# Kernel optimization log

Hardware: AMD Instinct MI355X
Metric: run time of the kernel (lower is better)

## Reference

```python
import jax, jax.numpy as jnp
import numpy as np

N_NODES = 50000
N_EDGES = 640000
HIDDEN = 128
N_LAYERS = 4
NUM_RBF = 50
CUTOFF = 4.0
N_GRAPHS = 64
VOCAB = 128
LN_EPS = 1e-5


def setup_inputs() -> dict:
    key = jax.random.key(0)
    ks = jax.random.split(key, 16)
    s = 1.0 / np.sqrt(HIDDEN)
    sr = 1.0 / np.sqrt(NUM_RBF)
    inp = {
        "x": jax.random.randint(ks[0], (N_NODES,), 0, VOCAB, dtype=jnp.int64) if jax.config.jax_enable_x64 else jax.random.randint(ks[0], (N_NODES,), 0, VOCAB).astype(jnp.int32),
        "edge_index": jax.random.randint(ks[1], (2, N_EDGES), 0, N_NODES).astype(jnp.int32),
        "edge_attr": jax.random.uniform(ks[2], (N_EDGES,), dtype=jnp.float32) * CUTOFF,
        "batch": jnp.sort(jax.random.randint(ks[3], (N_NODES,), 0, N_GRAPHS)).astype(jnp.int32),
        # embedding table
        "emb": jax.random.normal(ks[4], (VOCAB, HIDDEN), dtype=jnp.float32),
        # filter net: Linear(num_rbf, H) -> ReLU -> Linear(H, H), stacked over layers
        "fw1": jax.random.normal(ks[5], (N_LAYERS, NUM_RBF, HIDDEN), dtype=jnp.float32) * sr,
        "fb1": jnp.zeros((N_LAYERS, HIDDEN), dtype=jnp.float32),
        "fw2": jax.random.normal(ks[6], (N_LAYERS, HIDDEN, HIDDEN), dtype=jnp.float32) * s,
        "fb2": jnp.zeros((N_LAYERS, HIDDEN), dtype=jnp.float32),
        # lin: Linear(H, H) per layer
        "lw": jax.random.normal(ks[7], (N_LAYERS, HIDDEN, HIDDEN), dtype=jnp.float32) * s,
        "lb": jnp.zeros((N_LAYERS, HIDDEN), dtype=jnp.float32),
        # LayerNorm params per layer
        "ln_g": jnp.ones((N_LAYERS, HIDDEN), dtype=jnp.float32),
        "ln_b": jnp.zeros((N_LAYERS, HIDDEN), dtype=jnp.float32),
    }
    return inp


def _gaussian_smearing(dist):
    offset = jnp.linspace(0.0, CUTOFF, NUM_RBF, dtype=jnp.float32)  # [R]
    coeff = -0.5 / (CUTOFF / (NUM_RBF - 1)) ** 2
    d = dist[:, None] - offset[None, :]  # [E, R]
    return jnp.exp(coeff * d * d)


def _layer_norm(h, g, b):
    mu = jnp.mean(h, axis=-1, keepdims=True)
    var = jnp.mean(jnp.square(h - mu), axis=-1, keepdims=True)
    return (h - mu) * jax.lax.rsqrt(var + LN_EPS) * g + b


def reference(x, edge_index, edge_attr, batch, emb, fw1, fb1, fw2, fb2, lw, lb, ln_g, ln_b):
    edge_rbf = _gaussian_smearing(edge_attr)          # [E, R]
    h = emb[x]                                        # [N, H]
    row, col = edge_index[0], edge_index[1]
    for i in range(N_LAYERS):
        # FilterNet(RBF): [E, H]
        w = jax.nn.relu(edge_rbf @ fw1[i] + fb1[i]) @ fw2[i] + fb2[i]
        xl = h @ lw[i] + lb[i]                        # [N, H]
        msg = xl[col] * w                             # gather + elementwise, [E, H]
        out = jax.ops.segment_sum(msg, row, num_segments=N_NODES)
        h = _layer_norm(h + out, ln_g[i], ln_b[i])
    # global mean pool over graphs
    sums = jax.ops.segment_sum(h, batch, num_segments=N_GRAPHS)      # [G, H]
    cnt = jax.ops.segment_sum(jnp.ones((N_NODES,), h.dtype), batch, num_segments=N_GRAPHS)
    return sums / jnp.maximum(cnt, 1.0)[:, None]
```

## Files before the change

### kernel.cpp

```cpp
#include <hip/hip_runtime.h>
#include <hip/hip_bf16.h>

#define N_NODES 50000
#define N_EDGES 640000
#define HIDDEN 128
#define N_LAYERS 4
#define NUM_RBF 50
#define CUTOFF 4.0f
#define N_GRAPHS 64
#define TAB 8192
#define TG 8
#define PSPLIT 16
#define COLBITS 17

typedef unsigned int uint;
typedef unsigned short ushort;
typedef __attribute__((ext_vector_type(8))) short bf16x8;
typedef __attribute__((ext_vector_type(4))) float f32x4;

__device__ inline ushort f2bf(float f) {
    uint u = __float_as_uint(f);
    uint r = (u + 0x7fffu + ((u >> 16) & 1u)) >> 16;
    return (ushort)r;
}
__device__ inline uint packbf(float lo, float hi) {
    return (uint)f2bf(lo) | ((uint)f2bf(hi) << 16);
}
__device__ inline float bflo(uint u) { return __uint_as_float(u << 16); }
__device__ inline float bfhi(uint u) { return __uint_as_float(u & 0xffff0000u); }

__global__ __launch_bounds__(128) void k_table(const float* __restrict__ fw1,
                                               const float* __restrict__ fb1,
                                               const float* __restrict__ fw2,
                                               const float* __restrict__ fb2,
                                               uint* __restrict__ ctab) {
    int bid = blockIdx.x;
    int layer = bid / (TAB / TG);
    int g0 = (bid % (TAB / TG)) * TG;
    int j = threadIdx.x;
    __shared__ float rbf[TG][NUM_RBF];
    __shared__ float wout[TG][HIDDEN];
    __shared__ float hid[TG][HIDDEN];
    for (int idx = j; idx < TG * NUM_RBF; idx += 128) {
        int gg = idx / NUM_RBF, r = idx % NUM_RBF;
        float d = (CUTOFF * (g0 + gg)) / (float)(TAB - 1);
        float offset = (CUTOFF * r) / (float)(NUM_RBF - 1);
        float delta = CUTOFF / (float)(NUM_RBF - 1);
        float coeff = -0.5f / (delta * delta);
        float t = d - offset;
        rbf[gg][r] = expf(coeff * t * t);
    }
    __syncthreads();
    const float* w1 = fw1 + layer * NUM_RBF * HIDDEN;
    float b1 = fb1[layer * HIDDEN + j];
    float acc[TG];
    #pragma unroll
    for (int gg = 0; gg < TG; gg++) acc[gg] = b1;
    for (int r = 0; r < NUM_RBF; r++) {
        float w = w1[r * HIDDEN + j];
        #pragma unroll
        for (int gg = 0; gg < TG; gg++) acc[gg] = fmaf(rbf[gg][r], w, acc[gg]);
    }
    #pragma unroll
    for (int gg = 0; gg < TG; gg++) hid[gg][j] = fmaxf(acc[gg], 0.0f);
    __syncthreads();
    const float* w2 = fw2 + layer * HIDDEN * HIDDEN;
    float b2 = fb2[layer * HIDDEN + j];
    float acc2[TG];
    #pragma unroll
    for (int gg = 0; gg < TG; gg++) acc2[gg] = b2;
    for (int k = 0; k < HIDDEN; k += 4) {
        float w0 = w2[(k + 0) * HIDDEN + j];
        float w1v = w2[(k + 1) * HIDDEN + j];
        float w2v = w2[(k + 2) * HIDDEN + j];
        float w3 = w2[(k + 3) * HIDDEN + j];
        #pragma unroll
        for (int gg = 0; gg < TG; gg++) {
            acc2[gg] = fmaf(hid[gg][k + 0], w0, acc2[gg]);
            acc2[gg] = fmaf(hid[gg][k + 1], w1v, acc2[gg]);
            acc2[gg] = fmaf(hid[gg][k + 2], w2v, acc2[gg]);
            acc2[gg] = fmaf(hid[gg][k + 3], w3, acc2[gg]);
        }
    }
    #pragma unroll
    for (int gg = 0; gg < TG; gg++) wout[gg][j] = acc2[gg];
    __syncthreads();
    for (int idx = j; idx < TG * 64; idx += 128) {
        int gg = idx >> 6, jp = idx & 63;
        ctab[((size_t)layer * TAB + g0 + gg) * 64 + jp] =
            packbf(wout[gg][2 * jp], wout[gg][2 * jp + 1]);
    }
}

__global__ void k_embed(const int* __restrict__ x, const float* __restrict__ emb,
                        ushort* __restrict__ hbf) {
    int idx = blockIdx.x * 256 + threadIdx.x;
    if (idx >= N_NODES * 32) return;
    int n = idx >> 5, q = idx & 31;
    float4 v = ((const float4*)emb)[x[n] * 32 + q];
    uint2 p;
    p.x = packbf(v.x, v.y);
    p.y = packbf(v.z, v.w);
    ((uint2*)hbf)[idx] = p;
}

__global__ void k_packw(const float* __restrict__ lw, uint4* __restrict__ pb) {
    int idx = blockIdx.x * 256 + threadIdx.x;
    if (idx >= N_LAYERS * 8 * 4 * 64) return;
    int lane = idx & 63;
    int kc = (idx >> 6) & 3;
    int nt = (idx >> 8) & 7;
    int layer = idx >> 11;
    int quad = lane >> 4, nl = lane & 15;
    int n = nt * 16 + nl;
    const float* w = lw + layer * HIDDEN * HIDDEN;
    uint r[4];
    #pragma unroll
    for (int jj = 0; jj < 4; jj++) {
        int k = kc * 32 + quad * 8 + 2 * jj;
        r[jj] = packbf(w[k * HIDDEN + n], w[(k + 1) * HIDDEN + n]);
    }
    uint4 o; o.x = r[0]; o.y = r[1]; o.z = r[2]; o.w = r[3];
    pb[idx] = o;
}

__global__ void k_count(const int* __restrict__ row, int* __restrict__ counts) {
    int e = blockIdx.x * 256 + threadIdx.x;
    if (e < N_EDGES) atomicAdd(&counts[row[e]], 1);
}

__global__ void k_scan1(const int* __restrict__ counts, int* __restrict__ partial,
                        int* __restrict__ blocksum) {
    int i = blockIdx.x * 256 + threadIdx.x;
    int v = (i < N_NODES) ? counts[i] : 0;
    int lane = threadIdx.x & 63;
    int wid = threadIdx.x >> 6;
    int s = v;
    #pragma unroll
    for (int off = 1; off < 64; off <<= 1) {
        int t = __shfl_up(s, off, 64);
        if (lane >= off) s += t;
    }
    __shared__ int wsum[4];
    if (lane == 63) wsum[wid] = s;
    __syncthreads();
    int woff = 0;
    for (int w = 0; w < wid; w++) woff += wsum[w];
    int incl = s + woff;
    if (i < N_NODES) partial[i] = incl - v;
    if (threadIdx.x == 255) blocksum[blockIdx.x] = incl;
}

__global__ void k_scan2(int* __restrict__ blocksum, int nblk) {
    int tid = threadIdx.x;
    int v = (tid < nblk) ? blocksum[tid] : 0;
    int lane = tid & 63, wid = tid >> 6;
    int s = v;
    #pragma unroll
    for (int off = 1; off < 64; off <<= 1) {
        int t = __shfl_up(s, off, 64);
        if (lane >= off) s += t;
    }
    __shared__ int wsum[4];
    if (lane == 63) wsum[wid] = s;
    __syncthreads();
    int woff = 0;
    for (int w = 0; w < wid; w++) woff += wsum[w];
    int incl = s + woff;
    if (tid < nblk) blocksum[tid] = incl - v;
}

__global__ void k_scan3(const int* __restrict__ partial, const int* __restrict__ blocksum,
                        int* __restrict__ offsets, int* __restrict__ cursor) {
    int i = blockIdx.x * 256 + threadIdx.x;
    if (i < N_NODES) {
        int o = partial[i] + blocksum[blockIdx.x];
        offsets[i] = o;
        cursor[i] = o;
    }
    if (i == 0) offsets[N_NODES] = N_EDGES;
}

__global__ void k_fill(const int* __restrict__ row, const int* __restrict__ col,
                       const float* __restrict__ eattr, int* __restrict__ cursor,
                       uint* __restrict__ meta) {
    int e = blockIdx.x * 256 + threadIdx.x;
    if (e >= N_EDGES) return;
    int r = row[e];
    int pos = atomicAdd(&cursor[r], 1);
    float t = eattr[e] * ((float)(TAB - 1) / CUTOFF);
    int gi = (int)(t + 0.5f);
    gi = min(max(gi, 0), TAB - 1);
    meta[pos] = (uint)col[e] | ((uint)gi << COLBITS);
}

__global__ __launch_bounds__(256) void k_xl(const ushort* __restrict__ hbf,
                                            const uint4* __restrict__ pb,
                                            const float* __restrict__ lb,
                                            ushort* __restrict__ xlb) {
    int wave = threadIdx.x >> 6, lane = threadIdx.x & 63;
    int m0 = (blockIdx.x * 4 + wave) * 16;
    if (m0 >= N_NODES) return;
    int quad = lane >> 4, ml = lane & 15;
    const ushort* arow = hbf + (size_t)(m0 + ml) * HIDDEN + quad * 8;
    bf16x8 a[4];
    #pragma unroll
    for (int kc = 0; kc < 4; kc++) a[kc] = *(const bf16x8*)(arow + kc * 32);
    #pragma unroll
    for (int nt = 0; nt < 8; nt++) {
        f32x4 acc = {0.f, 0.f, 0.f, 0.f};
        #pragma unroll
        for (int kc = 0; kc < 4; kc++) {
            bf16x8 b = *(const bf16x8*)(pb + (nt * 4 + kc) * 64 + lane);
            acc = __builtin_amdgcn_mfma_f32_16x16x32_bf16(a[kc], b, acc, 0, 0, 0);
        }
        int col = nt * 16 + ml;
        float bias = lb[col];
        #pragma unroll
        for (int r = 0; r < 4; r++) {
            int row = m0 + quad * 4 + r;
            xlb[(size_t)row * HIDDEN + col] = f2bf(acc[r] + bias);
        }
    }
}

__global__ __launch_bounds__(256) void k_agg(const ushort* __restrict__ xlb,
                                             const uint* __restrict__ meta,
                                             const int* __restrict__ offsets,
                                             const uint* __restrict__ ctab,
                                             const ushort* __restrict__ hb_in,
                                             const float* __restrict__ g,
                                             const float* __restrict__ b,
                                             ushort* __restrict__ hbf_out) {
    int wid = threadIdx.x >> 6;
    int lane = threadIdx.x & 63;
    int n = blockIdx.x * 4 + wid;
    if (n >= N_NODES) return;
    const uint* xl2 = (const uint*)xlb;
    float accx = 0.f, accy = 0.f;
    int p0 = offsets[n], p1 = offsets[n + 1];
    int cnt = p1 - p0;
    for (int base = 0; base < cnt; base += 64) {
        int li = p0 + base + lane;
        uint mlv = meta[min(li, N_EDGES - 1)];
        int kk = min(64, cnt - base);
        int k4 = kk & ~3;
        int p = 0;
        for (; p < k4; p += 4) {
            uint m0 = __builtin_amdgcn_readlane(mlv, p + 0);
            uint m1 = __builtin_amdgcn_readlane(mlv, p + 1);
            uint m2 = __builtin_amdgcn_readlane(mlv, p + 2);
            uint m3 = __builtin_amdgcn_readlane(mlv, p + 3);
            uint w0 = ctab[(m0 >> COLBITS) * 64 + lane];
            uint w1 = ctab[(m1 >> COLBITS) * 64 + lane];
            uint w2 = ctab[(m2 >> COLBITS) * 64 + lane];
            uint w3 = ctab[(m3 >> COLBITS) * 64 + lane];
            uint x0 = xl2[(m0 & ((1u << COLBITS) - 1)) * 64 + lane];
            uint x1 = xl2[(m1 & ((1u << COLBITS) - 1)) * 64 + lane];
            uint x2 = xl2[(m2 & ((1u << COLBITS) - 1)) * 64 + lane];
            uint x3 = xl2[(m3 & ((1u << COLBITS) - 1)) * 64 + lane];
            accx = fmaf(bflo(w0), bflo(x0), accx);
            accy = fmaf(bfhi(w0), bfhi(x0), accy);
            accx = fmaf(bflo(w1), bflo(x1), accx);
            accy = fmaf(bfhi(w1), bfhi(x1), accy);
            accx = fmaf(bflo(w2), bflo(x2), accx);
            accy = fmaf(bfhi(w2), bfhi(x2), accy);
            accx = fmaf(bflo(w3), bflo(x3), accx);
            accy = fmaf(bfhi(w3), bfhi(x3), accy);
        }
        for (; p < kk; p++) {
            uint m = __builtin_amdgcn_readlane(mlv, p);
            uint w = ctab[(m >> COLBITS) * 64 + lane];
            uint xv = xl2[(m & ((1u << COLBITS) - 1)) * 64 + lane];
            accx = fmaf(bflo(w), bflo(xv), accx);
            accy = fmaf(bfhi(w), bfhi(xv), accy);
        }
    }
    uint hvp = ((const uint*)hb_in)[n * 64 + lane];
    float vx = bflo(hvp) + accx, vy = bfhi(hvp) + accy;
    float s = vx + vy;
    #pragma unroll
    for (int off = 32; off; off >>= 1) s += __shfl_xor(s, off, 64);
    float mu = s * (1.0f / 128.0f);
    float dx = vx - mu, dy = vy - mu;
    float s2 = dx * dx + dy * dy;
    #pragma unroll
    for (int off = 32; off; off >>= 1) s2 += __shfl_xor(s2, off, 64);
    float rstd = rsqrtf(s2 * (1.0f / 128.0f) + 1e-5f);
    float2 gv = ((const float2*)g)[lane];
    float2 bv = ((const float2*)b)[lane];
    float ox = fmaf(dx * rstd, gv.x, bv.x);
    float oy = fmaf(dy * rstd, gv.y, bv.y);
    ((uint*)hbf_out)[n * 64 + lane] = packbf(ox, oy);
}

__global__ void k_bounds(const int* __restrict__ batch, int* __restrict__ gstart) {
    int g = threadIdx.x;
    if (g > N_GRAPHS) return;
    int lo = 0, hi = N_NODES;
    while (lo < hi) {
        int mid = (lo + hi) >> 1;
        if (batch[mid] < g) lo = mid + 1; else hi = mid;
    }
    gstart[g] = lo;
}

__global__ __launch_bounds__(256) void k_pool_part(const ushort* __restrict__ hbf,
                                                   const int* __restrict__ gstart,
                                                   float* __restrict__ partial) {
    int g = blockIdx.x / PSPLIT;
    int t = blockIdx.x % PSPLIT;
    int jp = threadIdx.x & 63;
    int half = threadIdx.x >> 6;
    int s = gstart[g], e = gstart[g + 1];
    float accx = 0.f, accy = 0.f;
    const uint* h2 = (const uint*)hbf;
    for (int n = s + t * 4 + half; n < e; n += PSPLIT * 4) {
        uint v = h2[n * 64 + jp];
        accx += bflo(v);
        accy += bfhi(v);
    }
    __shared__ float redx[256], redy[256];
    redx[threadIdx.x] = accx;
    redy[threadIdx.x] = accy;
    __syncthreads();
    if (half == 0) {
        float tx = redx[jp] + redx[jp + 64] + redx[jp + 128] + redx[jp + 192];
        float ty = redy[jp] + redy[jp + 64] + redy[jp + 128] + redy[jp + 192];
        float2 o; o.x = tx; o.y = ty;
        ((float2*)partial)[(g * PSPLIT + t) * 64 + jp] = o;
    }
}

__global__ void k_pool_fin(const float* __restrict__ partial,
                           const int* __restrict__ gstart,
                           float* __restrict__ out) {
    int idx = blockIdx.x * 128 + threadIdx.x;
    int g = idx >> 7, j = idx & 127;
    float tot = 0.f;
    #pragma unroll
    for (int t = 0; t < PSPLIT; t++) tot += partial[(g * PSPLIT + t) * HIDDEN + j];
    float c = (float)(gstart[g + 1] - gstart[g]);
    out[idx] = tot / fmaxf(c, 1.0f);
}

extern "C" void kernel_launch(void* const* d_in, const int* in_sizes, int n_in,
                              void* d_out, int out_size, void* d_ws, size_t ws_size,
                              hipStream_t stream) {
    const int* x = (const int*)d_in[0];
    const int* edge_index = (const int*)d_in[1];
    const int* row = edge_index;
    const int* col = edge_index + N_EDGES;
    const float* eattr = (const float*)d_in[2];
    const int* batch = (const int*)d_in[3];
    const float* emb = (const float*)d_in[4];
    const float* fw1 = (const float*)d_in[5];
    const float* fb1 = (const float*)d_in[6];
    const float* fw2 = (const float*)d_in[7];
    const float* fb2 = (const float*)d_in[8];
    const float* lw = (const float*)d_in[9];
    const float* lb = (const float*)d_in[10];
    const float* ln_g = (const float*)d_in[11];
    const float* ln_b = (const float*)d_in[12];
    float* out = (float*)d_out;

    char* ws = (char*)d_ws;
    size_t off = 0;
    auto alloc = [&](size_t bytes) -> void* {
        void* p = ws + off;
        off = (off + bytes + 255) & ~(size_t)255;
        return p;
    };
    uint* ctab     = (uint*)alloc((size_t)N_LAYERS * TAB * 64 * 4);
    ushort* hbf_a  = (ushort*)alloc((size_t)N_NODES * HIDDEN * 2);
    ushort* hbf_b  = (ushort*)alloc((size_t)N_NODES * HIDDEN * 2);
    ushort* xlb    = (ushort*)alloc((size_t)N_NODES * HIDDEN * 2);
    uint4* pb      = (uint4*)alloc((size_t)N_LAYERS * 8 * 4 * 64 * 16);
    int* counts    = (int*)alloc((size_t)(N_NODES + 1) * 4);
    int* offsets   = (int*)alloc((size_t)(N_NODES + 1) * 4);
    int* cursor    = (int*)alloc((size_t)N_NODES * 4);
    int* partial   = (int*)alloc((size_t)N_NODES * 4);
    int* blocksum  = (int*)alloc(256 * 4);
    uint* meta     = (uint*)alloc((size_t)N_EDGES * 4);
    int* gstart    = (int*)alloc((size_t)(N_GRAPHS + 1) * 4);
    float* ppart   = (float*)alloc((size_t)N_GRAPHS * PSPLIT * HIDDEN * 4);

    hipMemsetAsync(counts, 0, (size_t)(N_NODES + 1) * 4, stream);

    k_table<<<N_LAYERS * (TAB / TG), 128, 0, stream>>>(fw1, fb1, fw2, fb2, ctab);
    k_embed<<<(N_NODES * 32 + 255) / 256, 256, 0, stream>>>(x, emb, hbf_a);
    k_packw<<<(N_LAYERS * 8 * 4 * 64 + 255) / 256, 256, 0, stream>>>(lw, pb);
    k_count<<<(N_EDGES + 255) / 256, 256, 0, stream>>>(row, counts);
    const int NBLK = (N_NODES + 255) / 256;
    k_scan1<<<NBLK, 256, 0, stream>>>(counts, partial, blocksum);
    k_scan2<<<1, 256, 0, stream>>>(blocksum, NBLK);
    k_scan3<<<NBLK, 256, 0, stream>>>(partial, blocksum, offsets, cursor);
    k_fill<<<(N_EDGES + 255) / 256, 256, 0, stream>>>(row, col, eattr, cursor, meta);
    k_bounds<<<1, 128, 0, stream>>>(batch, gstart);

    ushort* hb_cur = hbf_a; ushort* hb_nxt = hbf_b;
    const int XLBLK = (N_NODES / 16 + 3) / 4;
    for (int i = 0; i < N_LAYERS; i++) {
        k_xl<<<XLBLK, 256, 0, stream>>>(hb_cur, pb + (size_t)i * 8 * 4 * 64,
                                        lb + i * HIDDEN, xlb);
        k_agg<<<(N_NODES + 3) / 4, 256, 0, stream>>>(xlb, meta, offsets,
                                                     ctab + (size_t)i * TAB * 64,
                                                     hb_cur, ln_g + i * HIDDEN,
                                                     ln_b + i * HIDDEN, hb_nxt);
        ushort* tb = hb_cur; hb_cur = hb_nxt; hb_nxt = tb;
    }
    k_pool_part<<<N_GRAPHS * PSPLIT, 256, 0, stream>>>(hb_cur, gstart, ppart);
    k_pool_fin<<<(N_GRAPHS * HIDDEN + 127) / 128, 128, 0, stream>>>(ppart, gstart, out);
}
```

Before: 418.7 us.

## Replace global-atomic CSR fill with two-pass bucketed counting sort

```diff
diff --git a/kernel.cpp b/kernel.cpp
--- a/kernel.cpp
+++ b/kernel.cpp
@@ -12,6 +12,8 @@
 #define TG 8
 #define PSPLIT 16
 #define COLBITS 17
+#define NBUCK 196
+#define CHUNK 4096
 
 typedef unsigned int uint;
 typedef unsigned short ushort;
@@ -171,27 +173,84 @@
 }
 
 __global__ void k_scan3(const int* __restrict__ partial, const int* __restrict__ blocksum,
-                        int* __restrict__ offsets, int* __restrict__ cursor) {
+                        int* __restrict__ offsets, int* __restrict__ bcur) {
     int i = blockIdx.x * 256 + threadIdx.x;
     if (i < N_NODES) {
         int o = partial[i] + blocksum[blockIdx.x];
         offsets[i] = o;
-        cursor[i] = o;
+        if ((i & 255) == 0) bcur[i >> 8] = o;
     }
     if (i == 0) offsets[N_NODES] = N_EDGES;
 }
 
-__global__ void k_fill(const int* __restrict__ row, const int* __restrict__ col,
-                       const float* __restrict__ eattr, int* __restrict__ cursor,
-                       uint* __restrict__ meta) {
-    int e = blockIdx.x * 256 + threadIdx.x;
-    if (e >= N_EDGES) return;
-    int r = row[e];
-    int pos = atomicAdd(&cursor[r], 1);
-    float t = eattr[e] * ((float)(TAB - 1) / CUTOFF);
-    int gi = (int)(t + 0.5f);
-    gi = min(max(gi, 0), TAB - 1);
-    meta[pos] = (uint)col[e] | ((uint)gi << COLBITS);
+__global__ __launch_bounds__(256) void k_bucket(const int* __restrict__ row,
+                                                const int* __restrict__ col,
+                                                const float* __restrict__ eattr,
+                                                int* __restrict__ bcur,
+                                                uint2* __restrict__ bs) {
+    __shared__ uint2 stage[CHUNK];
+    __shared__ int hist[256], lscan[256], lcur[256], gbase[256];
+    __shared__ int wsum[4];
+    int t = threadIdx.x;
+    int e0 = blockIdx.x * CHUNK;
+    int ne = min(CHUNK, N_EDGES - e0);
+    hist[t] = 0;
+    __syncthreads();
+    for (int i = t; i < ne; i += 256)
+        atomicAdd(&hist[row[e0 + i] >> 8], 1);
+    __syncthreads();
+    int v = hist[t];
+    int lane = t & 63, wid = t >> 6;
+    int s = v;
+    #pragma unroll
+    for (int off = 1; off < 64; off <<= 1) {
+        int u = __shfl_up(s, off, 64);
+        if (lane >= off) s += u;
+    }
+    if (lane == 63) wsum[wid] = s;
+    __syncthreads();
+    int woff = 0;
+    for (int w = 0; w < wid; w++) woff += wsum[w];
+    int excl = s + woff - v;
+    lscan[t] = excl;
+    lcur[t] = excl;
+    if (v > 0) gbase[t] = atomicAdd(&bcur[t], v);
+    __syncthreads();
+    for (int i = t; i < ne; i += 256) {
+        int e = e0 + i;
+        int r = row[e];
+        float tt = eattr[e] * ((float)(TAB - 1) / CUTOFF);
+        int gi = (int)(tt + 0.5f);
+        gi = min(max(gi, 0), TAB - 1);
+        int pos = atomicAdd(&lcur[r >> 8], 1);
+        uint2 sv;
+        sv.x = (uint)col[e] | ((uint)gi << COLBITS);
+        sv.y = (uint)r;
+        stage[pos] = sv;
+    }
+    __syncthreads();
+    for (int i = t; i < ne; i += 256) {
+        uint2 sv = stage[i];
+        int b = sv.y >> 8;
+        bs[gbase[b] + (i - lscan[b])] = sv;
+    }
+}
+
+__global__ __launch_bounds__(256) void k_scatter(const uint2* __restrict__ bs,
+                                                 const int* __restrict__ offsets,
+                                                 uint* __restrict__ meta) {
+    int b = blockIdx.x, t = threadIdx.x;
+    int r0 = b << 8;
+    __shared__ int cur[256];
+    int rmax = min(r0 + 256, N_NODES);
+    cur[t] = offsets[min(r0 + t, N_NODES)];
+    __syncthreads();
+    int s = offsets[r0], e = offsets[rmax];
+    for (int i = s + t; i < e; i += 256) {
+        uint2 v = bs[i];
+        int slot = atomicAdd(&cur[v.y - r0], 1);
+        meta[slot] = v.x;
+    }
 }
 
 __global__ __launch_bounds__(256) void k_xl(const ushort* __restrict__ hbf,
@@ -378,9 +437,10 @@
     uint4* pb      = (uint4*)alloc((size_t)N_LAYERS * 8 * 4 * 64 * 16);
     int* counts    = (int*)alloc((size_t)(N_NODES + 1) * 4);
     int* offsets   = (int*)alloc((size_t)(N_NODES + 1) * 4);
-    int* cursor    = (int*)alloc((size_t)N_NODES * 4);
     int* partial   = (int*)alloc((size_t)N_NODES * 4);
     int* blocksum  = (int*)alloc(256 * 4);
+    int* bcur      = (int*)alloc(256 * 4);
+    uint2* bs      = (uint2*)alloc((size_t)N_EDGES * 8);
     uint* meta     = (uint*)alloc((size_t)N_EDGES * 4);
     int* gstart    = (int*)alloc((size_t)(N_GRAPHS + 1) * 4);
     float* ppart   = (float*)alloc((size_t)N_GRAPHS * PSPLIT * HIDDEN * 4);
@@ -394,8 +454,9 @@
     const int NBLK = (N_NODES + 255) / 256;
     k_scan1<<<NBLK, 256, 0, stream>>>(counts, partial, blocksum);
     k_scan2<<<1, 256, 0, stream>>>(blocksum, NBLK);
-    k_scan3<<<NBLK, 256, 0, stream>>>(partial, blocksum, offsets, cursor);
-    k_fill<<<(N_EDGES + 255) / 256, 256, 0, stream>>>(row, col, eattr, cursor, meta);
+    k_scan3<<<NBLK, 256, 0, stream>>>(partial, blocksum, offsets, bcur);
+    k_bucket<<<(N_EDGES + CHUNK - 1) / CHUNK, 256, 0, stream>>>(row, col, eattr, bcur, bs);
+    k_scatter<<<NBUCK, 256, 0, stream>>>(bs, offsets, meta);
     k_bounds<<<1, 128, 0, stream>>>(batch, gstart);
 
     ushort* hb_cur = hbf_a; ushort* hb_nxt = hbf_b;
```

After: 401.7 us. 4.1% less time.
